# Optimization experiments

Measured on AMD Instinct MI355X. Metric: run time of the kernel, lower is better.

## Reference

```python
import jax, jax.numpy as jnp
import numpy as np

H = 256          # hidden_dim from config
B, S = 128, 2048 # batch, seq_len
D_CTX, D_RFX = 6, 2


def setup_inputs() -> dict:
    key = jax.random.key(0)
    ks = jax.random.split(key, 16)
    def lin(k, out_d, in_d):
        # torch nn.Linear default init: U(-1/sqrt(in_d), 1/sqrt(in_d))
        bound = 1.0 / np.sqrt(in_d)
        k1, k2 = jax.random.split(k)
        w = jax.random.uniform(k1, (out_d, in_d), jnp.float32, -bound, bound)
        b = jax.random.uniform(k2, (out_d,), jnp.float32, -bound, bound)
        return w, b
    x = jax.random.normal(ks[0], (B, S, D_CTX), jnp.float32)
    # GRUCell params (torch layout: rows ordered [reset, update, new])
    bnd = 1.0 / np.sqrt(H)
    w_ih = jax.random.uniform(ks[1], (3 * H, D_CTX), jnp.float32, -bnd, bnd)
    w_hh = jax.random.uniform(ks[2], (3 * H, H), jnp.float32, -bnd, bnd)
    b_ih = jax.random.uniform(ks[3], (3 * H,), jnp.float32, -bnd, bnd)
    b_hh = jax.random.uniform(ks[4], (3 * H,), jnp.float32, -bnd, bnd)
    w_gain, b_gain = lin(ks[5], D_RFX, H)
    w_bias, b_bias = lin(ks[6], 4, H)
    w_reflex, b_reflex = lin(ks[7], H, D_RFX)
    w_policy, b_policy = lin(ks[8], 2, H)
    w_motor, b_motor = lin(ks[9], 2, H)
    return dict(x=x, w_ih=w_ih, w_hh=w_hh, b_ih=b_ih, b_hh=b_hh,
                w_gain=w_gain, b_gain=b_gain, w_bias=w_bias, b_bias=b_bias,
                w_reflex=w_reflex, b_reflex=b_reflex,
                w_policy=w_policy, b_policy=b_policy,
                w_motor=w_motor, b_motor=b_motor)


def _forward(x, w_ih, w_hh, b_ih, b_hh, w_gain, b_gain, w_bias, b_bias,
             w_reflex, b_reflex, w_policy, b_policy, w_motor, b_motor):
    # x_context == cat(x[:,:,0:2], x[:,:,2:3], x[:,:,3:6]) == x itself
    x_reflex = x[:, :, 0:2]
    # Precompute input contribution to all 3 GRU gates: [B, S, 3H]
    gates_x = jnp.einsum('bsd,gd->bsg', x, w_ih) + b_ih
    gates_x_t = jnp.swapaxes(gates_x, 0, 1)     # [S, B, 3H]
    x_reflex_t = jnp.swapaxes(x_reflex, 0, 1)   # [S, B, 2]

    h0 = jnp.zeros((x.shape[0], H), x.dtype)

    def step(h, inp):
        gi, xr = inp
        gh = h @ w_hh.T + b_hh
        r = jax.nn.sigmoid(gi[:, :H] + gh[:, :H])
        z = jax.nn.sigmoid(gi[:, H:2 * H] + gh[:, H:2 * H])
        n = jnp.tanh(gi[:, 2 * H:] + r * gh[:, 2 * H:])
        h_new = (1.0 - z) * n + z * h
        gain = jax.nn.sigmoid(h_new @ w_gain.T + b_gain)   # [B,2]
        bias = h_new @ w_bias.T + b_bias                    # [B,4]
        feat = jax.nn.relu((xr * gain) @ w_reflex.T + b_reflex)  # [B,H]
        probs = feat @ w_policy.T + b_policy + bias[:, 0:2]
        dirs = jnp.tanh(feat @ w_motor.T + b_motor + bias[:, 2:4])
        y = jnp.concatenate([probs, dirs], axis=1)          # [B,4]
        return h_new, (y, h_new)

    _, (y_t, h_t) = jax.lax.scan(step, h0, (gates_x_t, x_reflex_t))
    y_pred = jnp.swapaxes(y_t, 0, 1)          # [B,S,4]
    router_activity = jnp.swapaxes(h_t, 0, 1) # [B,S,H]
    return y_pred, router_activity


def reference(x, w_ih, w_hh, b_ih, b_hh, w_gain, b_gain, w_bias, b_bias,
              w_reflex, b_reflex, w_policy, b_policy, w_motor, b_motor):
    return _forward(x, w_ih, w_hh, b_ih, b_hh, w_gain, b_gain, w_bias, b_bias,
                    w_reflex, b_reflex, w_policy, b_policy, w_motor, b_motor)
```

## Files before the change

### kernel.cpp

```cpp
#include <hip/hip_runtime.h>
#include <cstdint>
#include <cstddef>

#define Hn 256
#define Sn 2048
#define Bn 128
#define NT 1024

typedef _Float16 half2_t __attribute__((ext_vector_type(2)));

__device__ __forceinline__ float fdot2_(half2_t a, half2_t b, float c){
#if __has_builtin(__builtin_amdgcn_fdot2)
  return __builtin_amdgcn_fdot2(a, b, c, false);
#else
  float d;
  asm volatile("v_dot2_f32_f16 %0, %1, %2, %3" : "=v"(d) : "v"(a), "v"(b), "v"(c));
  return d;
#endif
}

__device__ __forceinline__ float qsum_(float v){
  int x = __builtin_bit_cast(int, v);
  int y = __builtin_amdgcn_mov_dpp(x, 0xB1, 0xF, 0xF, true);
  v += __builtin_bit_cast(float, y);
  x = __builtin_bit_cast(int, v);
  y = __builtin_amdgcn_mov_dpp(x, 0x4E, 0xF, 0xF, true);
  return v + __builtin_bit_cast(float, y);
}

__device__ __forceinline__ float rfl_(float v){
  return __builtin_bit_cast(float, __builtin_amdgcn_readfirstlane(__builtin_bit_cast(int, v)));
}

__device__ __forceinline__ float sigmoid_(float v){ return 1.0f/(1.0f+__expf(-v)); }
__device__ __forceinline__ float tanh_(float v){
  float e = __expf(-2.0f*__builtin_fabsf(v));
  float r = (1.0f-e)/(1.0f+e);
  return __builtin_copysignf(r, v);
}

__global__ void __launch_bounds__(NT, 1)
bio_rnn(const float* __restrict__ x,
        const float* __restrict__ w_ih, const float* __restrict__ w_hh,
        const float* __restrict__ b_ih, const float* __restrict__ b_hh,
        const float* __restrict__ w_gain, const float* __restrict__ b_gain,
        const float* __restrict__ w_bias, const float* __restrict__ b_bias,
        const float* __restrict__ w_reflex, const float* __restrict__ b_reflex,
        const float* __restrict__ w_policy, const float* __restrict__ b_policy,
        const float* __restrict__ w_motor, const float* __restrict__ b_motor,
        float* __restrict__ y_out, float* __restrict__ router)
{
  const int b  = blockIdx.x;
  const int t  = threadIdx.x;
  const int kq = t & 3;
  const int j  = t >> 2;

  __shared__ __align__(16) unsigned char hraw[4*160];
  __shared__ float PRE[4][Hn];
  __shared__ float REDp[4][8];
  __shared__ float REDq[4][4];
  __shared__ float HW[13][Hn];
  __shared__ float SB[10];

  half2_t w0[32], w1[32], w2[32];
  {
    const float* p0 = w_hh + (size_t)(j       )*Hn + kq*64;
    const float* p1 = w_hh + (size_t)(j +   Hn)*Hn + kq*64;
    const float* p2 = w_hh + (size_t)(j + 2*Hn)*Hn + kq*64;
    #pragma unroll
    for (int m = 0; m < 32; m++){
      half2_t a; a.x=(_Float16)p0[2*m]; a.y=(_Float16)p0[2*m+1]; w0[m]=a;
      half2_t c; c.x=(_Float16)p1[2*m]; c.y=(_Float16)p1[2*m+1]; w1[m]=c;
      half2_t d; d.x=(_Float16)p2[2*m]; d.y=(_Float16)p2[2*m+1]; w2[m]=d;
    }
  }
  half2_t wi0, wi1, wi2; float bd0, bd1, bd2, bd3;
  {
    half2_t z; z.x=(_Float16)0.f; z.y=(_Float16)0.f;
    wi0=z; wi1=z; wi2=z; bd0=bd1=bd2=bd3=0.f;
    if (kq < 3){
      wi0.x=(_Float16)w_ih[(size_t)(j       )*6+2*kq]; wi0.y=(_Float16)w_ih[(size_t)(j       )*6+2*kq+1];
      wi1.x=(_Float16)w_ih[(size_t)(j +   Hn)*6+2*kq]; wi1.y=(_Float16)w_ih[(size_t)(j +   Hn)*6+2*kq+1];
      wi2.x=(_Float16)w_ih[(size_t)(j + 2*Hn)*6+2*kq]; wi2.y=(_Float16)w_ih[(size_t)(j + 2*Hn)*6+2*kq+1];
    } else {
      bd0 = b_ih[j]      + b_hh[j];
      bd1 = b_ih[j+Hn]   + b_hh[j+Hn];
      bd2 = b_hh[j+2*Hn];
      bd3 = b_ih[j+2*Hn];
    }
  }
  if (t < Hn){
    HW[0][t] = w_gain[t];        HW[1][t]  = w_gain[Hn + t];
    HW[2][t] = w_bias[t];        HW[3][t]  = w_bias[Hn + t];
    HW[4][t] = w_bias[2*Hn + t]; HW[5][t]  = w_bias[3*Hn + t];
    HW[6][t] = w_reflex[2*t];    HW[7][t]  = w_reflex[2*t + 1];
    HW[8][t] = b_reflex[t];
    HW[9][t] = w_policy[t];      HW[10][t] = w_policy[Hn + t];
    HW[11][t] = w_motor[t];      HW[12][t] = w_motor[Hn + t];
  }
  if (t < 160) ((unsigned int*)hraw)[t] = 0u;
  if (t == 0){
    SB[0]=b_gain[0]; SB[1]=b_gain[1];
    SB[2]=b_bias[0]; SB[3]=b_bias[1]; SB[4]=b_bias[2]; SB[5]=b_bias[3];
    SB[6]=b_policy[0]; SB[7]=b_policy[1]; SB[8]=b_motor[0]; SB[9]=b_motor[1];
  }
  float hprev = 0.f;
  __syncthreads();

  const float* xp   = x      + (size_t)b * Sn * 6;
  float* rbase      = router + (size_t)b * Sn * Hn;
  const uint4* hc   = (const uint4*)(hraw + kq*160);

  for (int s = 0; s < Sn; s++){
    const float x0=rfl_(xp[0]), x1=rfl_(xp[1]), x2=rfl_(xp[2]);
    const float x3=rfl_(xp[3]), x4=rfl_(xp[4]), x5=rfl_(xp[5]);
    float xa = (kq==0)?x0:((kq==1)?x2:x4);
    float xb = (kq==0)?x1:((kq==1)?x3:x5);
    half2_t xpk; xpk.x=(_Float16)xa; xpk.y=(_Float16)xb;

    float a0=bd0, a1=bd1, a2=bd2, a3=bd3;
    a0 = fdot2_(wi0, xpk, a0);
    a1 = fdot2_(wi1, xpk, a1);
    a3 = fdot2_(wi2, xpk, a3);

    #pragma unroll
    for (int i = 0; i < 8; i++){
      uint4 hv = hc[i];
      half2_t h0 = __builtin_bit_cast(half2_t, hv.x);
      half2_t h1 = __builtin_bit_cast(half2_t, hv.y);
      half2_t h2 = __builtin_bit_cast(half2_t, hv.z);
      half2_t h3 = __builtin_bit_cast(half2_t, hv.w);
      a0=fdot2_(w0[4*i+0],h0,a0); a1=fdot2_(w1[4*i+0],h0,a1); a2=fdot2_(w2[4*i+0],h0,a2);
      a0=fdot2_(w0[4*i+1],h1,a0); a1=fdot2_(w1[4*i+1],h1,a1); a2=fdot2_(w2[4*i+1],h1,a2);
      a0=fdot2_(w0[4*i+2],h2,a0); a1=fdot2_(w1[4*i+2],h2,a1); a2=fdot2_(w2[4*i+2],h2,a2);
      a0=fdot2_(w0[4*i+3],h3,a0); a1=fdot2_(w1[4*i+3],h3,a1); a2=fdot2_(w2[4*i+3],h3,a2);
    }
    a0 = qsum_(a0); a1 = qsum_(a1); a2 = qsum_(a2); a3 = qsum_(a3);
    if (kq == 0){ PRE[0][j]=a0; PRE[1][j]=a1; PRE[2][j]=a2; PRE[3][j]=a3; }
    __syncthreads();

    if (t < Hn){
      float pr = PRE[0][t], pz = PRE[1][t], pg = PRE[2][t], pn = PRE[3][t];
      float r = sigmoid_(pr);
      float z = sigmoid_(pz);
      float n = tanh_(pn + r*pg);
      float h = (1.f - z)*n + z*hprev;
      hprev = h;
      *(_Float16*)(hraw + (t>>6)*160 + (t&63)*2) = (_Float16)h;
      rbase[(size_t)s*Hn + t] = h;
      float p0=h*HW[0][t], p1=h*HW[1][t], p2=h*HW[2][t];
      float p3=h*HW[3][t], p4=h*HW[4][t], p5=h*HW[5][t];
      #pragma unroll
      for (int off = 32; off >= 1; off >>= 1){
        p0 += __shfl_xor(p0, off); p1 += __shfl_xor(p1, off); p2 += __shfl_xor(p2, off);
        p3 += __shfl_xor(p3, off); p4 += __shfl_xor(p4, off); p5 += __shfl_xor(p5, off);
      }
      if ((t & 63) == 0){
        const int wv = t >> 6;
        REDp[wv][0]=p0; REDp[wv][1]=p1; REDp[wv][2]=p2;
        REDp[wv][3]=p3; REDp[wv][4]=p4; REDp[wv][5]=p5;
      }
    }
    __syncthreads();
    if (t < Hn){
      float g0 = REDp[0][0]+REDp[1][0]+REDp[2][0]+REDp[3][0] + SB[0];
      float g1 = REDp[0][1]+REDp[1][1]+REDp[2][1]+REDp[3][1] + SB[1];
      g0 = sigmoid_(g0); g1 = sigmoid_(g1);
      float f = (x0*g0)*HW[6][t] + (x1*g1)*HW[7][t] + HW[8][t];
      f = fmaxf(f, 0.f);
      float q0=f*HW[9][t], q1=f*HW[10][t], q2=f*HW[11][t], q3=f*HW[12][t];
      #pragma unroll
      for (int off = 32; off >= 1; off >>= 1){
        q0 += __shfl_xor(q0, off); q1 += __shfl_xor(q1, off);
        q2 += __shfl_xor(q2, off); q3 += __shfl_xor(q3, off);
      }
      if ((t & 63) == 0){
        const int wv = t >> 6;
        REDq[wv][0]=q0; REDq[wv][1]=q1; REDq[wv][2]=q2; REDq[wv][3]=q3;
      }
    }
    __syncthreads();
    if (t == 0){
      float s0 = REDq[0][0]+REDq[1][0]+REDq[2][0]+REDq[3][0];
      float s1 = REDq[0][1]+REDq[1][1]+REDq[2][1]+REDq[3][1];
      float s2 = REDq[0][2]+REDq[1][2]+REDq[2][2]+REDq[3][2];
      float s3 = REDq[0][3]+REDq[1][3]+REDq[2][3]+REDq[3][3];
      float B0 = REDp[0][2]+REDp[1][2]+REDp[2][2]+REDp[3][2] + SB[2];
      float B1 = REDp[0][3]+REDp[1][3]+REDp[2][3]+REDp[3][3] + SB[3];
      float B2 = REDp[0][4]+REDp[1][4]+REDp[2][4]+REDp[3][4] + SB[4];
      float B3 = REDp[0][5]+REDp[1][5]+REDp[2][5]+REDp[3][5] + SB[5];
      float4 o;
      o.x = s0 + SB[6] + B0;
      o.y = s1 + SB[7] + B1;
      o.z = tanh_(s2 + SB[8] + B2);
      o.w = tanh_(s3 + SB[9] + B3);
      *(float4*)(y_out + (size_t)b * Sn * 4 + (size_t)s * 4) = o;
    }
    xp += 6;
  }
}

extern "C" void kernel_launch(void* const* d_in, const int* in_sizes, int n_in,
                              void* d_out, int out_size, void* d_ws, size_t ws_size,
                              hipStream_t stream)
{
  const float* x        = (const float*)d_in[0];
  const float* w_ih     = (const float*)d_in[1];
  const float* w_hh     = (const float*)d_in[2];
  const float* b_ih     = (const float*)d_in[3];
  const float* b_hh     = (const float*)d_in[4];
  const float* w_gain   = (const float*)d_in[5];
  const float* b_gain   = (const float*)d_in[6];
  const float* w_bias   = (const float*)d_in[7];
  const float* b_bias   = (const float*)d_in[8];
  const float* w_reflex = (const float*)d_in[9];
  const float* b_reflex = (const float*)d_in[10];
  const float* w_policy = (const float*)d_in[11];
  const float* b_policy = (const float*)d_in[12];
  const float* w_motor  = (const float*)d_in[13];
  const float* b_motor  = (const float*)d_in[14];

  float* y_out  = (float*)d_out;
  float* router = (float*)d_out + (size_t)Bn * Sn * 4;

  bio_rnn<<<dim3(Bn), dim3(NT), 0, stream>>>(
      x, w_ih, w_hh, b_ih, b_hh, w_gain, b_gain, w_bias, b_bias,
      w_reflex, b_reflex, w_policy, b_policy, w_motor, b_motor,
      y_out, router);
}
```

Measured before the change: 6.341 ms.

## Split recurrent weights across AGPRs, VGPRs and LDS and use DPP row reductions

The per-thread fp16 recurrent weights are now split across three places. The reset and update gate weights sit in accumulation registers (AGPRs), read with v_accvgpr_read. Half of the new-gate weights stay in VGPRs and the other half are staged in a large LDS array. This frees architectural VGPRs, likely to avoid spilling or register pressure at 1024 threads, and the launch bound's min-blocks hint is dropped. The wave reductions also switch from shfl_xor butterflies to DPP row_shr/row_bcast scans, and the weight conversions use cvt_pkrtz. The risks are extra LDS reads and AGPR-read latency inside the serial step loop.

```diff
diff --git a/kernel.cpp b/kernel.cpp
--- a/kernel.cpp
+++ b/kernel.cpp
@@ -8,6 +8,8 @@
 #define NT 1024
 
 typedef _Float16 half2_t __attribute__((ext_vector_type(2)));
+
+__device__ __forceinline__ half2_t bc2_(unsigned int u){ return __builtin_bit_cast(half2_t, u); }
 
 __device__ __forceinline__ float fdot2_(half2_t a, half2_t b, float c){
 #if __has_builtin(__builtin_amdgcn_fdot2)
@@ -19,6 +21,14 @@
 #endif
 }
 
+__device__ __forceinline__ float rfl_(float v){
+  return __builtin_bit_cast(float, __builtin_amdgcn_readfirstlane(__builtin_bit_cast(int, v)));
+}
+
+__device__ __forceinline__ half2_t pkrtz_(float a, float b){
+  return __builtin_bit_cast(half2_t, __builtin_amdgcn_cvt_pkrtz(a, b));
+}
+
 __device__ __forceinline__ float qsum_(float v){
   int x = __builtin_bit_cast(int, v);
   int y = __builtin_amdgcn_mov_dpp(x, 0xB1, 0xF, 0xF, true);
@@ -28,8 +38,21 @@
   return v + __builtin_bit_cast(float, y);
 }
 
-__device__ __forceinline__ float rfl_(float v){
-  return __builtin_bit_cast(float, __builtin_amdgcn_readfirstlane(__builtin_bit_cast(int, v)));
+__device__ __forceinline__ float wsum_(float v){
+  int x;
+  x = __builtin_amdgcn_update_dpp(0, __builtin_bit_cast(int, v), 0x111, 0xF, 0xF, false);
+  v += __builtin_bit_cast(float, x);
+  x = __builtin_amdgcn_update_dpp(0, __builtin_bit_cast(int, v), 0x112, 0xF, 0xF, false);
+  v += __builtin_bit_cast(float, x);
+  x = __builtin_amdgcn_update_dpp(0, __builtin_bit_cast(int, v), 0x114, 0xF, 0xF, false);
+  v += __builtin_bit_cast(float, x);
+  x = __builtin_amdgcn_update_dpp(0, __builtin_bit_cast(int, v), 0x118, 0xF, 0xF, false);
+  v += __builtin_bit_cast(float, x);
+  x = __builtin_amdgcn_update_dpp(0, __builtin_bit_cast(int, v), 0x142, 0xA, 0xF, false);
+  v += __builtin_bit_cast(float, x);
+  x = __builtin_amdgcn_update_dpp(0, __builtin_bit_cast(int, v), 0x143, 0xC, 0xF, false);
+  v += __builtin_bit_cast(float, x);
+  return v;
 }
 
 __device__ __forceinline__ float sigmoid_(float v){ return 1.0f/(1.0f+__expf(-v)); }
@@ -39,7 +62,11 @@
   return __builtin_copysignf(r, v);
 }
 
-__global__ void __launch_bounds__(NT, 1)
+#define F32_(M) M(0) M(1) M(2) M(3) M(4) M(5) M(6) M(7) M(8) M(9) M(10) M(11) \
+  M(12) M(13) M(14) M(15) M(16) M(17) M(18) M(19) M(20) M(21) M(22) M(23) \
+  M(24) M(25) M(26) M(27) M(28) M(29) M(30) M(31)
+
+__global__ void __launch_bounds__(NT)
 bio_rnn(const float* __restrict__ x,
         const float* __restrict__ w_ih, const float* __restrict__ w_hh,
         const float* __restrict__ b_ih, const float* __restrict__ b_hh,
@@ -55,6 +82,7 @@
   const int kq = t & 3;
   const int j  = t >> 2;
 
+  __shared__ unsigned int WL[NT * 20];
   __shared__ __align__(16) unsigned char hraw[4*160];
   __shared__ float PRE[4][Hn];
   __shared__ float REDp[4][8];
@@ -62,26 +90,40 @@
   __shared__ float HW[13][Hn];
   __shared__ float SB[10];
 
-  half2_t w0[32], w1[32], w2[32];
+#define DAG(i) unsigned agr##i, agz##i;
+  F32_(DAG)
+#undef DAG
   {
-    const float* p0 = w_hh + (size_t)(j       )*Hn + kq*64;
-    const float* p1 = w_hh + (size_t)(j +   Hn)*Hn + kq*64;
-    const float* p2 = w_hh + (size_t)(j + 2*Hn)*Hn + kq*64;
+    const float* wrR = w_hh + (size_t)(j      )*Hn + kq*64;
+    const float* wrZ = w_hh + (size_t)(j + Hn )*Hn + kq*64;
+#define WAG(i) { unsigned pr = __builtin_bit_cast(unsigned, pkrtz_(wrR[2*i], wrR[2*i+1])); \
+                 unsigned pz = __builtin_bit_cast(unsigned, pkrtz_(wrZ[2*i], wrZ[2*i+1])); \
+                 asm("v_accvgpr_write_b32 %0, %1" : "=a"(agr##i) : "v"(pr)); \
+                 asm("v_accvgpr_write_b32 %0, %1" : "=a"(agz##i) : "v"(pz)); }
+    F32_(WAG)
+#undef WAG
+  }
+  uint4 WR0, WR1, WR2, WR3;
+  {
+    const float* wrN = w_hh + (size_t)(j + 2*Hn)*Hn + kq*64;
+#define PK(m) __builtin_bit_cast(unsigned, pkrtz_(wrN[2*(m)], wrN[2*(m)+1]))
+    WR0 = (uint4){PK(0),PK(1),PK(2),PK(3)};
+    WR1 = (uint4){PK(4),PK(5),PK(6),PK(7)};
+    WR2 = (uint4){PK(8),PK(9),PK(10),PK(11)};
+    WR3 = (uint4){PK(12),PK(13),PK(14),PK(15)};
     #pragma unroll
-    for (int m = 0; m < 32; m++){
-      half2_t a; a.x=(_Float16)p0[2*m]; a.y=(_Float16)p0[2*m+1]; w0[m]=a;
-      half2_t c; c.x=(_Float16)p1[2*m]; c.y=(_Float16)p1[2*m+1]; w1[m]=c;
-      half2_t d; d.x=(_Float16)p2[2*m]; d.y=(_Float16)p2[2*m+1]; w2[m]=d;
-    }
+    for (int i = 0; i < 16; i++)
+      WL[t*20 + i] = __builtin_bit_cast(unsigned, pkrtz_(wrN[32+2*i], wrN[32+2*i+1]));
+#undef PK
   }
   half2_t wi0, wi1, wi2; float bd0, bd1, bd2, bd3;
   {
     half2_t z; z.x=(_Float16)0.f; z.y=(_Float16)0.f;
     wi0=z; wi1=z; wi2=z; bd0=bd1=bd2=bd3=0.f;
     if (kq < 3){
-      wi0.x=(_Float16)w_ih[(size_t)(j       )*6+2*kq]; wi0.y=(_Float16)w_ih[(size_t)(j       )*6+2*kq+1];
-      wi1.x=(_Float16)w_ih[(size_t)(j +   Hn)*6+2*kq]; wi1.y=(_Float16)w_ih[(size_t)(j +   Hn)*6+2*kq+1];
-      wi2.x=(_Float16)w_ih[(size_t)(j + 2*Hn)*6+2*kq]; wi2.y=(_Float16)w_ih[(size_t)(j + 2*Hn)*6+2*kq+1];
+      wi0 = pkrtz_(w_ih[(size_t)(j       )*6+2*kq], w_ih[(size_t)(j       )*6+2*kq+1]);
+      wi1 = pkrtz_(w_ih[(size_t)(j +  Hn )*6+2*kq], w_ih[(size_t)(j +  Hn )*6+2*kq+1]);
+      wi2 = pkrtz_(w_ih[(size_t)(j + 2*Hn)*6+2*kq], w_ih[(size_t)(j + 2*Hn)*6+2*kq+1]);
     } else {
       bd0 = b_ih[j]      + b_hh[j];
       bd1 = b_ih[j+Hn]   + b_hh[j+Hn];
@@ -109,32 +151,47 @@
 
   const float* xp   = x      + (size_t)b * Sn * 6;
   float* rbase      = router + (size_t)b * Sn * Hn;
-  const uint4* hc   = (const uint4*)(hraw + kq*160);
+  const uint4* hc4  = (const uint4*)(hraw + kq*160);
+  const uint4* WLv  = (const uint4*)WL;
+
+#define GCH(c, nv_, r0,r1,r2,r3) { \
+    const uint4 Hc = hc4[c]; const uint4 Nw = (nv_); \
+    unsigned u0,u1,u2,u3,v0,v1,v2,v3; \
+    asm("v_accvgpr_read_b32 %0, %1" : "=v"(u0) : "a"(agr##r0)); \
+    asm("v_accvgpr_read_b32 %0, %1" : "=v"(u1) : "a"(agr##r1)); \
+    asm("v_accvgpr_read_b32 %0, %1" : "=v"(u2) : "a"(agr##r2)); \
+    asm("v_accvgpr_read_b32 %0, %1" : "=v"(u3) : "a"(agr##r3)); \
+    asm("v_accvgpr_read_b32 %0, %1" : "=v"(v0) : "a"(agz##r0)); \
+    asm("v_accvgpr_read_b32 %0, %1" : "=v"(v1) : "a"(agz##r1)); \
+    asm("v_accvgpr_read_b32 %0, %1" : "=v"(v2) : "a"(agz##r2)); \
+    asm("v_accvgpr_read_b32 %0, %1" : "=v"(v3) : "a"(agz##r3)); \
+    a0=fdot2_(bc2_(u0),bc2_(Hc.x),a0); a1=fdot2_(bc2_(v0),bc2_(Hc.x),a1); a2=fdot2_(bc2_(Nw.x),bc2_(Hc.x),a2); \
+    a0=fdot2_(bc2_(u1),bc2_(Hc.y),a0); a1=fdot2_(bc2_(v1),bc2_(Hc.y),a1); a2=fdot2_(bc2_(Nw.y),bc2_(Hc.y),a2); \
+    a0=fdot2_(bc2_(u2),bc2_(Hc.z),a0); a1=fdot2_(bc2_(v2),bc2_(Hc.z),a1); a2=fdot2_(bc2_(Nw.z),bc2_(Hc.z),a2); \
+    a0=fdot2_(bc2_(u3),bc2_(Hc.w),a0); a1=fdot2_(bc2_(v3),bc2_(Hc.w),a1); a2=fdot2_(bc2_(Nw.w),bc2_(Hc.w),a2); }
 
   for (int s = 0; s < Sn; s++){
     const float x0=rfl_(xp[0]), x1=rfl_(xp[1]), x2=rfl_(xp[2]);
     const float x3=rfl_(xp[3]), x4=rfl_(xp[4]), x5=rfl_(xp[5]);
     float xa = (kq==0)?x0:((kq==1)?x2:x4);
     float xb = (kq==0)?x1:((kq==1)?x3:x5);
-    half2_t xpk; xpk.x=(_Float16)xa; xpk.y=(_Float16)xb;
-
-    float a0=bd0, a1=bd1, a2=bd2, a3=bd3;
-    a0 = fdot2_(wi0, xpk, a0);
-    a1 = fdot2_(wi1, xpk, a1);
-    a3 = fdot2_(wi2, xpk, a3);
-
-    #pragma unroll
-    for (int i = 0; i < 8; i++){
-      uint4 hv = hc[i];
-      half2_t h0 = __builtin_bit_cast(half2_t, hv.x);
-      half2_t h1 = __builtin_bit_cast(half2_t, hv.y);
-      half2_t h2 = __builtin_bit_cast(half2_t, hv.z);
-      half2_t h3 = __builtin_bit_cast(half2_t, hv.w);
-      a0=fdot2_(w0[4*i+0],h0,a0); a1=fdot2_(w1[4*i+0],h0,a1); a2=fdot2_(w2[4*i+0],h0,a2);
-      a0=fdot2_(w0[4*i+1],h1,a0); a1=fdot2_(w1[4*i+1],h1,a1); a2=fdot2_(w2[4*i+1],h1,a2);
-      a0=fdot2_(w0[4*i+2],h2,a0); a1=fdot2_(w1[4*i+2],h2,a1); a2=fdot2_(w2[4*i+2],h2,a2);
-      a0=fdot2_(w0[4*i+3],h3,a0); a1=fdot2_(w1[4*i+3],h3,a1); a2=fdot2_(w2[4*i+3],h3,a2);
-    }
+    half2_t xpk = pkrtz_(xa, xb);
+
+    float a0 = fdot2_(wi0, xpk, bd0);
+    float a1 = fdot2_(wi1, xpk, bd1);
+    float a2 = bd2;
+    float a3 = fdot2_(wi2, xpk, bd3);
+
+    const int wlb = t*5;
+    GCH(0, WR0,  0, 1, 2, 3)
+    GCH(1, WR1,  4, 5, 6, 7)
+    GCH(2, WR2,  8, 9,10,11)
+    GCH(3, WR3, 12,13,14,15)
+    GCH(4, WLv[wlb+0], 16,17,18,19)
+    GCH(5, WLv[wlb+1], 20,21,22,23)
+    GCH(6, WLv[wlb+2], 24,25,26,27)
+    GCH(7, WLv[wlb+3], 28,29,30,31)
+
     a0 = qsum_(a0); a1 = qsum_(a1); a2 = qsum_(a2); a3 = qsum_(a3);
     if (kq == 0){ PRE[0][j]=a0; PRE[1][j]=a1; PRE[2][j]=a2; PRE[3][j]=a3; }
     __syncthreads();
@@ -148,14 +205,13 @@
       hprev = h;
       *(_Float16*)(hraw + (t>>6)*160 + (t&63)*2) = (_Float16)h;
       rbase[(size_t)s*Hn + t] = h;
-      float p0=h*HW[0][t], p1=h*HW[1][t], p2=h*HW[2][t];
-      float p3=h*HW[3][t], p4=h*HW[4][t], p5=h*HW[5][t];
-      #pragma unroll
-      for (int off = 32; off >= 1; off >>= 1){
-        p0 += __shfl_xor(p0, off); p1 += __shfl_xor(p1, off); p2 += __shfl_xor(p2, off);
-        p3 += __shfl_xor(p3, off); p4 += __shfl_xor(p4, off); p5 += __shfl_xor(p5, off);
-      }
-      if ((t & 63) == 0){
+      float p0 = wsum_(h*HW[0][t]);
+      float p1 = wsum_(h*HW[1][t]);
+      float p2 = wsum_(h*HW[2][t]);
+      float p3 = wsum_(h*HW[3][t]);
+      float p4 = wsum_(h*HW[4][t]);
+      float p5 = wsum_(h*HW[5][t]);
+      if ((t & 63) == 63){
         const int wv = t >> 6;
         REDp[wv][0]=p0; REDp[wv][1]=p1; REDp[wv][2]=p2;
         REDp[wv][3]=p3; REDp[wv][4]=p4; REDp[wv][5]=p5;
@@ -168,13 +224,11 @@
       g0 = sigmoid_(g0); g1 = sigmoid_(g1);
       float f = (x0*g0)*HW[6][t] + (x1*g1)*HW[7][t] + HW[8][t];
       f = fmaxf(f, 0.f);
-      float q0=f*HW[9][t], q1=f*HW[10][t], q2=f*HW[11][t], q3=f*HW[12][t];
-      #pragma unroll
-      for (int off = 32; off >= 1; off >>= 1){
-        q0 += __shfl_xor(q0, off); q1 += __shfl_xor(q1, off);
-        q2 += __shfl_xor(q2, off); q3 += __shfl_xor(q3, off);
-      }
-      if ((t & 63) == 0){
+      float q0 = wsum_(f*HW[9][t]);
+      float q1 = wsum_(f*HW[10][t]);
+      float q2 = wsum_(f*HW[11][t]);
+      float q3 = wsum_(f*HW[12][t]);
+      if ((t & 63) == 63){
         const int wv = t >> 6;
         REDq[wv][0]=q0; REDq[wv][1]=q1; REDq[wv][2]=q2; REDq[wv][3]=q3;
       }
@@ -198,6 +252,7 @@
     }
     xp += 6;
   }
+#undef GCH
 }
 
 extern "C" void kernel_launch(void* const* d_in, const int* in_sizes, int n_in,
```

Result: no change. 6.467 ms (+2.0%).
